# Kernel optimization log

Hardware: AMD Instinct MI355X
Metric: run time of the kernel (lower is better)

The kernel has to match this reference:

```python
import jax, jax.numpy as jnp
import numpy as np


def _elem_mlp(x, w1, b1, w2, b2):
    # elementwise 1 -> N -> 1 ReLU MLP (distilled exp / inv approximators)
    h = jax.nn.relu(x[..., None] * w1[:, 0] + b1)  # [..., N]
    return jnp.einsum('...n,n->...', h, w2[0]) + b2[0]


def setup_inputs() -> dict:
    key = jax.random.key(0)
    ks = jax.random.split(key, 13)
    T, S, B, D = 8, 512, 8, 512
    NE, NI = 32, 64
    f = jnp.float32
    inp = {
        'sx': jax.random.normal(ks[0], (T, S, B, D), f) * 0.1,
        'q_proj_weight': jax.random.normal(ks[1], (D, D), f) / np.sqrt(D),
        'k_proj_weight': jax.random.normal(ks[2], (D, D), f) / np.sqrt(D),
        'q_proj_bias': jax.random.normal(ks[3], (D,), f) * 0.02,
        'k_proj_bias': jax.random.normal(ks[4], (D,), f) * 0.02,
        'exp_w1': jax.random.normal(ks[5], (NE, 1), f),
        'exp_b1': jax.random.normal(ks[6], (NE,), f) * 0.1,
        'exp_w2': jax.random.normal(ks[7], (1, NE), f) / np.sqrt(NE),
        'exp_b2': jax.random.normal(ks[8], (1,), f) * 0.01,
        'inv_w1': jax.random.normal(ks[9], (NI, 1), f),
        'inv_b1': jax.random.normal(ks[10], (NI,), f) * 0.1,
        'inv_w2': jax.random.normal(ks[11], (1, NI), f) / np.sqrt(NI),
        'inv_b2': jax.random.normal(ks[12], (1,), f) * 0.01,
        'num_heads': 8,
    }
    return inp


def reference(sx, q_proj_weight, k_proj_weight, q_proj_bias, k_proj_bias,
              exp_w1, exp_b1, exp_w2, exp_b2,
              inv_w1, inv_b1, inv_w2, inv_b2, num_heads):
    T, S, B, D = sx.shape
    H = num_heads
    hd = D // H
    scale = 1.0 / np.sqrt(hd)

    def proj(x_t, W, b):
        # [S, B, D] -> [B*H, S, hd]
        y = x_t @ W.T + b
        return y.reshape(S, B * H, hd).transpose(1, 0, 2)

    def step(carry, x_t):
        sum_q, sum_k, sum_p = carry
        sq = proj(x_t, q_proj_weight, q_proj_bias)
        sk = proj(x_t, k_proj_weight, k_proj_bias)
        sum_q = sum_q + sq
        # sp_t = sum_q @ sk^T + sq @ sum_k^T (sum_k updated AFTER, per snn_qk_product)
        sp = (jnp.einsum('bsh,bth->bst', sum_q, sk)
              + jnp.einsum('bsh,bth->bst', sq, sum_k)) * scale
        sum_k = sum_k + sk
        return (sum_q, sum_k, sum_p + sp), None

    z_qk = jnp.zeros((B * H, S, hd), sx.dtype)
    z_p = jnp.zeros((B * H, S, S), sx.dtype)
    (sum_q, sum_k, sum_p), _ = jax.lax.scan(step, (z_qk, z_qk, z_p), sx)

    p = sum_p / T  # time-averaged accumulated QK product

    # fit_softmax: distilled-MLP softmax approximation
    tmax = p[:, :, 0:1]
    tp = jnp.minimum(p - (tmax - 1.0), 3.0)
    x_up = jnp.where(tp > -20.0,
                     _elem_mlp(tp, exp_w1, exp_b1, exp_w2, exp_b2), 0.0)
    partition = x_up.sum(-1, keepdims=True)
    p_inv = _elem_mlp(partition, inv_w1, inv_b1, inv_w2, inv_b2)
    out = x_up * p_inv
    partition_p2 = out.sum(-1, keepdims=True)
    p_inv2 = _elem_mlp(partition_p2, inv_w1, inv_b1, inv_w2, inv_b2)
    out2 = jnp.where(partition_p2 > 1.5, out * p_inv2, out)
    return out2
```

## Files before the change

kernel.cpp:

```cpp
#include <hip/hip_runtime.h>


#define T_  8
#define NE_ 32
#define NI_ 64

#define LUT_N   2048
#define LUT_LO  -20.0f
#define LUT_HI  3.0f
#define LUT_INVW (LUT_N / (LUT_HI - LUT_LO))
#define LUT_W    ((LUT_HI - LUT_LO) / LUT_N)

typedef __attribute__((ext_vector_type(8))) short bf16x8;
typedef __attribute__((ext_vector_type(4))) float f32x4;
typedef __attribute__((ext_vector_type(4))) unsigned int u32x4;

#define XS_OFF 0u
#define WQ_OFF 2097152u
#define WK_OFF 2359296u
#define QB_OFF 2621440u
#define KB_OFF 4718592u
#define LUT_OFF 6815744u

__device__ inline unsigned short f2bf(float f) {
  union { float f; unsigned u; } v; v.f = f;
  unsigned r = v.u + 0x7FFFu + ((v.u >> 16) & 1u);
  return (unsigned short)(r >> 16);
}

__device__ inline void gload16(const void* g, void* l) {
  __builtin_amdgcn_global_load_lds(
      (const __attribute__((address_space(1))) void*)g,
      (__attribute__((address_space(3))) void*)l, 16, 0, 0);
}

__device__ inline bf16x8 lds_read_swz(const unsigned short* base, int row, int byteoff) {
  int addr = row * 128 + (byteoff ^ ((row & 7) << 4));
  return *(const bf16x8*)((const char*)base + addr);
}

__device__ inline float invmlp4(float x, const float* __restrict__ w1,
                                const float* __restrict__ b1,
                                const float* __restrict__ w2, float b2) {
  float a0 = b2, a1 = 0.f, a2 = 0.f, a3 = 0.f;
#pragma unroll
  for (int n = 0; n < NI_; n += 4) {
    a0 += w2[n + 0] * fmaxf(x * w1[n + 0] + b1[n + 0], 0.0f);
    a1 += w2[n + 1] * fmaxf(x * w1[n + 1] + b1[n + 1], 0.0f);
    a2 += w2[n + 2] * fmaxf(x * w1[n + 2] + b1[n + 2], 0.0f);
    a3 += w2[n + 3] * fmaxf(x * w1[n + 3] + b1[n + 3], 0.0f);
  }
  return (a0 + a1) + (a2 + a3);
}

__device__ inline float expmlp_exact(float t, const float* __restrict__ w1,
                                     const float* __restrict__ b1,
                                     const float* __restrict__ w2, float b2) {
  float a = b2;
#pragma unroll
  for (int n = 0; n < NE_; n++) a += w2[n] * fmaxf(t * w1[n] + b1[n], 0.0f);
  return a;
}

__global__ __launch_bounds__(256) void k_pre(
    const float* __restrict__ sx, const float* __restrict__ wq,
    const float* __restrict__ wk, const float* __restrict__ ew1,
    const float* __restrict__ eb1, const float* __restrict__ ew2,
    const float* __restrict__ eb2p,
    unsigned short* __restrict__ xs, unsigned short* __restrict__ wqb,
    unsigned short* __restrict__ wkb, float2* __restrict__ lut) {
  int bx = blockIdx.x, tid = threadIdx.x;
  if (bx < 2048) {
    size_t i = ((size_t)bx * 256 + tid) * 4;
    f32x4 a = __builtin_nontemporal_load((const f32x4*)(sx + i));
#pragma unroll
    for (int t = 1; t < T_; t++) {
      f32x4 v = __builtin_nontemporal_load((const f32x4*)(sx + (size_t)t * 2097152 + i));
      a += v;
    }
    ushort4 o; o.x = f2bf(a[0]); o.y = f2bf(a[1]); o.z = f2bf(a[2]); o.w = f2bf(a[3]);
    *(ushort4*)(xs + i) = o;
  } else if (bx < 2560) {
    const float* src = (bx < 2304) ? wq : wk;
    unsigned short* dst = (bx < 2304) ? wqb : wkb;
    int base = (bx < 2304) ? 2048 : 2304;
    size_t i = ((size_t)(bx - base) * 256 + tid) * 4;
    float4 a = *(const float4*)(src + i);
    ushort4 o; o.x = f2bf(a.x); o.y = f2bf(a.y); o.z = f2bf(a.z); o.w = f2bf(a.w);
    *(ushort4*)(dst + i) = o;
  } else {
    int i = (bx - 2560) * 256 + tid;
    if (i < LUT_N) {
      float b2 = eb2p[0];
      float tl = fmaf((float)i, LUT_W, LUT_LO);
      float th = fmaf((float)(i + 1), LUT_W, LUT_LO);
      float el = expmlp_exact(tl, ew1, eb1, ew2, b2);
      float eh = expmlp_exact(th, ew1, eb1, ew2, b2);
      float ap = eh - el;
      float bp = fmaf(-ap, (float)i, el);
      lut[i] = make_float2(ap, bp);
    }
  }
}

__global__ __launch_bounds__(256, 2) void k_proj(
    const unsigned short* __restrict__ xs, const unsigned short* __restrict__ wb,
    const float* __restrict__ bq, const float* __restrict__ bk,
    unsigned short* __restrict__ outb) {
  __shared__ unsigned short As[64 * 64];
  __shared__ unsigned short Bs[128 * 64];
  int tid = threadIdx.x;
  int lane = tid & 63, w = tid >> 6;
  int r0 = blockIdx.x * 64;
  int c0 = blockIdx.y * 128;
  int z = blockIdx.z;
  const unsigned short* W = wb + (size_t)z * 262144;
  const float* bias = z ? bk : bq;
  unsigned short* dst = outb + (size_t)z * 2097152;
  float sc = z ? 1.0f : (1.0f / 64.0f);

  int rgrp = lane >> 4, cl = lane & 15;
  int r0w = (w >> 1) * 32, c0w = (w & 1) * 64;

  f32x4 acc[2][4];
  f32x4 zero = {0.f, 0.f, 0.f, 0.f};
#pragma unroll
  for (int m = 0; m < 2; m++)
#pragma unroll
    for (int n = 0; n < 4; n++) acc[m][n] = zero;

  int rl = lane >> 3, slot = lane & 7;

  for (int kt = 0; kt < 8; kt++) {
    int k0 = kt * 64;
#pragma unroll
    for (int i = 0; i < 2; i++) {
      int chunk = w * 2 + i;
      int r = chunk * 8 + rl;
      int sw = (slot ^ (r & 7)) * 8;
      gload16(xs + (size_t)(r0 + r) * 512 + k0 + sw, (char*)As + chunk * 1024);
    }
#pragma unroll
    for (int i = 0; i < 4; i++) {
      int chunk = w * 4 + i;
      int r = chunk * 8 + rl;
      int sw = (slot ^ (r & 7)) * 8;
      gload16(W + (size_t)(c0 + r) * 512 + k0 + sw, (char*)Bs + chunk * 1024);
    }
    __syncthreads();
#pragma unroll
    for (int kb = 0; kb < 2; kb++) {
      bf16x8 af[2], bfr[4];
#pragma unroll
      for (int m = 0; m < 2; m++) af[m] = lds_read_swz(As, r0w + 16 * m + cl, kb * 64 + rgrp * 16);
#pragma unroll
      for (int n = 0; n < 4; n++) bfr[n] = lds_read_swz(Bs, c0w + 16 * n + cl, kb * 64 + rgrp * 16);
#pragma unroll
      for (int m = 0; m < 2; m++)
#pragma unroll
        for (int n = 0; n < 4; n++)
          acc[m][n] = __builtin_amdgcn_mfma_f32_16x16x32_bf16(af[m], bfr[n], acc[m][n], 0, 0, 0);
    }
    __syncthreads();
  }

  unsigned short* Os = Bs;
#pragma unroll
  for (int n = 0; n < 4; n++) {
    int cgl = c0w + 16 * n + cl;
    float bv = 8.0f * bias[c0 + cgl];
    int hl = cgl >> 6, dh = cgl & 63;
    int hh = dh >> 5, rg2 = (dh >> 3) & 3, jj = dh & 7;
#pragma unroll
    for (int m = 0; m < 2; m++) {
#pragma unroll
      for (int j = 0; j < 4; j++) {
        int rgl = r0w + 16 * m + rgrp * 4 + j;
        int b = rgl & 7, clsl = rgl >> 3;
        Os[((((b * 2 + hl) * 2 + hh) * 4 + rg2) * 8 + clsl) * 8 + jj] =
            f2bf((acc[m][n][j] + bv) * sc);
      }
    }
  }
  __syncthreads();

  int cb = blockIdx.x >> 1;
  int clsbase = (blockIdx.x & 1) * 8;
  int h0 = c0 >> 6;
#pragma unroll
  for (int i2 = 0; i2 < 4; i2++) {
    int unit = i2 * 256 + tid;
    int clsl = unit & 7, rg2 = (unit >> 3) & 3, hh = (unit >> 5) & 1;
    int hl = (unit >> 6) & 1, b = unit >> 7;
    int bh = b * 8 + h0 + hl;
    size_t du = ((size_t)((bh * 32 + cb) * 2 + hh)) * 512 + (rg2 * 16 + clsbase + clsl) * 8;
    *(u32x4*)(dst + du) = *(const u32x4*)(Os + unit * 8);
  }
}

__global__ __launch_bounds__(256, 4) void k_attn(
    const unsigned short* __restrict__ qb, const unsigned short* __restrict__ kb,
    const float2* __restrict__ lutg,
    const float* __restrict__ iw1, const float* __restrict__ ib1,
    const float* __restrict__ iw2, const float* __restrict__ ib2p,
    float* __restrict__ out) {
  __shared__ float2 Lut[LUT_N];
  __shared__ float s_part[4][16];
  __shared__ float s_fac[16];

  int tid = threadIdx.x;
  int lane = tid & 63, w = tid >> 6;
  int i = blockIdx.x;
  int xcd = i & 7, j2 = i >> 3;
  int bh = xcd * 8 + (j2 >> 5);
  int rb = j2 & 31;
  int rgrp = lane >> 4, cl = lane & 15;

#pragma unroll
  for (int c = 0; c < 4; c++) {
    int chunk = w * 4 + c;
    gload16((const char*)lutg + chunk * 1024 + lane * 16, (char*)Lut + chunk * 1024);
  }

  const char* Qb = (const char*)qb + (size_t)((bh * 32 + rb) * 2) * 1024;
  bf16x8 aF0 = *(const bf16x8*)(Qb + lane * 16);
  bf16x8 aF1 = *(const bf16x8*)(Qb + 1024 + lane * 16);

  const char* Kbase = (const char*)kb + (size_t)(bh * 32) * 2048;
  f32x4 zero = {0.f, 0.f, 0.f, 0.f};

  float tm1[4];
  {
    bf16x8 b0 = *(const bf16x8*)(Kbase + lane * 16);
    bf16x8 b1 = *(const bf16x8*)(Kbase + 1024 + lane * 16);
    f32x4 p0 = __builtin_amdgcn_mfma_f32_16x16x32_bf16(aF0, b0, zero, 0, 0, 0);
    p0 = __builtin_amdgcn_mfma_f32_16x16x32_bf16(aF1, b1, p0, 0, 0, 0);
    int src = lane & 48;
#pragma unroll
    for (int j = 0; j < 4; j++) tm1[j] = __shfl(p0[j], src) - 1.0f;
  }

  f32x4 acc[8];
#pragma unroll
  for (int f = 0; f < 8; f++) {
    const char* Kb = Kbase + (size_t)(w * 8 + f) * 2048;
    bf16x8 b0 = *(const bf16x8*)(Kb + lane * 16);
    bf16x8 b1 = *(const bf16x8*)(Kb + 1024 + lane * 16);
    acc[f] = __builtin_amdgcn_mfma_f32_16x16x32_bf16(aF0, b0, zero, 0, 0, 0);
    acc[f] = __builtin_amdgcn_mfma_f32_16x16x32_bf16(aF1, b1, acc[f], 0, 0, 0);
  }

  __syncthreads();

  const float C0 = -LUT_LO * LUT_INVW;
  float cj[4];
#pragma unroll
  for (int j = 0; j < 4; j++) cj[j] = fmaf(-tm1[j], LUT_INVW, C0);

  float rowsum[4] = {0.f, 0.f, 0.f, 0.f};
#pragma unroll
  for (int f = 0; f < 8; f++) {
#pragma unroll
    for (int j = 0; j < 4; j++) {
      float u0 = fmaf(acc[f][j], LUT_INVW, cj[j]);
      float u = fminf(fmaxf(u0, 0.0f), (float)LUT_N);
      int bi = (int)u;
      bi = min(bi, LUT_N - 1);
      float2 ab = Lut[bi];
      float xu = fmaf(ab.x, u, ab.y);
      xu = (u0 > 0.0f) ? xu : 0.0f;
      acc[f][j] = xu;
      rowsum[j] += xu;
    }
  }

#pragma unroll
  for (int j = 0; j < 4; j++) {
    float s = rowsum[j];
    s += __shfl_xor(s, 1);
    s += __shfl_xor(s, 2);
    s += __shfl_xor(s, 4);
    s += __shfl_xor(s, 8);
    if (cl == 0) s_part[w][rgrp * 4 + j] = s;
  }
  __syncthreads();

  if (tid < 16) {
    float part = s_part[0][tid] + s_part[1][tid] + s_part[2][tid] + s_part[3][tid];
    float b2 = ib2p[0];
    float fac = invmlp4(part, iw1, ib1, iw2, b2);
    float pp2 = part * fac;
    if (pp2 > 1.5f) fac *= invmlp4(pp2, iw1, ib1, iw2, b2);
    s_fac[tid] = fac;
  }
  __syncthreads();

  float* outb = out + ((size_t)bh * 512 + rb * 16) * 512;
#pragma unroll
  for (int j = 0; j < 4; j++) {
    int row = rgrp * 4 + j;
    float fac = s_fac[row];
#pragma unroll
    for (int f = 0; f < 8; f++)
      __builtin_nontemporal_store(acc[f][j] * fac,
          &outb[(size_t)row * 512 + w * 128 + 16 * f + cl]);
  }
}

extern "C" void kernel_launch(void* const* d_in, const int* in_sizes, int n_in,
                              void* d_out, int out_size, void* d_ws, size_t ws_size,
                              hipStream_t stream) {
  (void)in_sizes; (void)n_in; (void)out_size; (void)ws_size;
  const float* sx  = (const float*)d_in[0];
  const float* wq  = (const float*)d_in[1];
  const float* wk  = (const float*)d_in[2];
  const float* bq  = (const float*)d_in[3];
  const float* bk  = (const float*)d_in[4];
  const float* ew1 = (const float*)d_in[5];
  const float* eb1 = (const float*)d_in[6];
  const float* ew2 = (const float*)d_in[7];
  const float* eb2 = (const float*)d_in[8];
  const float* iw1 = (const float*)d_in[9];
  const float* ib1 = (const float*)d_in[10];
  const float* iw2 = (const float*)d_in[11];
  const float* ib2 = (const float*)d_in[12];
  unsigned short* wsu = (unsigned short*)d_ws;
  float2* lut = (float2*)(wsu + LUT_OFF);
  float* out = (float*)d_out;

  k_pre<<<2568, 256, 0, stream>>>(sx, wq, wk, ew1, eb1, ew2, eb2,
                                  wsu + XS_OFF, wsu + WQ_OFF, wsu + WK_OFF, lut);
  k_proj<<<dim3(64, 4, 2), 256, 0, stream>>>(wsu + XS_OFF, wsu + WQ_OFF, bq, bk, wsu + QB_OFF);
  k_attn<<<2048, 256, 0, stream>>>(wsu + QB_OFF, wsu + KB_OFF, lut,
                                   iw1, ib1, iw2, ib2, out);
}
```

Baseline: 56.62 us.

## Transpose QK MFMA operands so each lane owns a row; vectorize stores, split inverse MLP

Swaps the A/B operands of the QK MFMA so each lane's four accumulator values belong to one query row across four adjacent columns, instead of four rows. The row max offset and row sum then each need one scalar per lane, and the sum reduces with two cross-lane shuffles instead of four per row. The inverse-MLP normalisation, previously run serially by 16 threads behind an extra barrier, is now split across all lanes with a shuffle reduction. This removes a __syncthreads and lets the output be written as 16-byte vector nontemporal stores. The trade-off is that every lane now computes the second inverse MLP whether or not the threshold is met.

```diff
diff --git a/kernel.cpp b/kernel.cpp
--- a/kernel.cpp
+++ b/kernel.cpp
@@ -37,20 +37,6 @@
 __device__ inline bf16x8 lds_read_swz(const unsigned short* base, int row, int byteoff) {
   int addr = row * 128 + (byteoff ^ ((row & 7) << 4));
   return *(const bf16x8*)((const char*)base + addr);
-}
-
-__device__ inline float invmlp4(float x, const float* __restrict__ w1,
-                                const float* __restrict__ b1,
-                                const float* __restrict__ w2, float b2) {
-  float a0 = b2, a1 = 0.f, a2 = 0.f, a3 = 0.f;
-#pragma unroll
-  for (int n = 0; n < NI_; n += 4) {
-    a0 += w2[n + 0] * fmaxf(x * w1[n + 0] + b1[n + 0], 0.0f);
-    a1 += w2[n + 1] * fmaxf(x * w1[n + 1] + b1[n + 1], 0.0f);
-    a2 += w2[n + 2] * fmaxf(x * w1[n + 2] + b1[n + 2], 0.0f);
-    a3 += w2[n + 3] * fmaxf(x * w1[n + 3] + b1[n + 3], 0.0f);
-  }
-  return (a0 + a1) + (a2 + a3);
 }
 
 __device__ inline float expmlp_exact(float t, const float* __restrict__ w1,
@@ -206,7 +192,6 @@
     float* __restrict__ out) {
   __shared__ float2 Lut[LUT_N];
   __shared__ float s_part[4][16];
-  __shared__ float s_fac[16];
 
   int tid = threadIdx.x;
   int lane = tid & 63, w = tid >> 6;
@@ -223,46 +208,42 @@
   }
 
   const char* Qb = (const char*)qb + (size_t)((bh * 32 + rb) * 2) * 1024;
-  bf16x8 aF0 = *(const bf16x8*)(Qb + lane * 16);
-  bf16x8 aF1 = *(const bf16x8*)(Qb + 1024 + lane * 16);
+  bf16x8 qF0 = *(const bf16x8*)(Qb + lane * 16);
+  bf16x8 qF1 = *(const bf16x8*)(Qb + 1024 + lane * 16);
 
   const char* Kbase = (const char*)kb + (size_t)(bh * 32) * 2048;
   f32x4 zero = {0.f, 0.f, 0.f, 0.f};
 
-  float tm1[4];
+  float tm1;
   {
-    bf16x8 b0 = *(const bf16x8*)(Kbase + lane * 16);
-    bf16x8 b1 = *(const bf16x8*)(Kbase + 1024 + lane * 16);
-    f32x4 p0 = __builtin_amdgcn_mfma_f32_16x16x32_bf16(aF0, b0, zero, 0, 0, 0);
-    p0 = __builtin_amdgcn_mfma_f32_16x16x32_bf16(aF1, b1, p0, 0, 0, 0);
-    int src = lane & 48;
-#pragma unroll
-    for (int j = 0; j < 4; j++) tm1[j] = __shfl(p0[j], src) - 1.0f;
+    bf16x8 k0 = *(const bf16x8*)(Kbase + lane * 16);
+    bf16x8 k1 = *(const bf16x8*)(Kbase + 1024 + lane * 16);
+    f32x4 p0 = __builtin_amdgcn_mfma_f32_16x16x32_bf16(k0, qF0, zero, 0, 0, 0);
+    p0 = __builtin_amdgcn_mfma_f32_16x16x32_bf16(k1, qF1, p0, 0, 0, 0);
+    tm1 = __shfl(p0[0], cl) - 1.0f;
   }
 
   f32x4 acc[8];
 #pragma unroll
   for (int f = 0; f < 8; f++) {
     const char* Kb = Kbase + (size_t)(w * 8 + f) * 2048;
-    bf16x8 b0 = *(const bf16x8*)(Kb + lane * 16);
-    bf16x8 b1 = *(const bf16x8*)(Kb + 1024 + lane * 16);
-    acc[f] = __builtin_amdgcn_mfma_f32_16x16x32_bf16(aF0, b0, zero, 0, 0, 0);
-    acc[f] = __builtin_amdgcn_mfma_f32_16x16x32_bf16(aF1, b1, acc[f], 0, 0, 0);
+    bf16x8 k0 = *(const bf16x8*)(Kb + lane * 16);
+    bf16x8 k1 = *(const bf16x8*)(Kb + 1024 + lane * 16);
+    acc[f] = __builtin_amdgcn_mfma_f32_16x16x32_bf16(k0, qF0, zero, 0, 0, 0);
+    acc[f] = __builtin_amdgcn_mfma_f32_16x16x32_bf16(k1, qF1, acc[f], 0, 0, 0);
   }
 
   __syncthreads();
 
   const float C0 = -LUT_LO * LUT_INVW;
-  float cj[4];
-#pragma unroll
-  for (int j = 0; j < 4; j++) cj[j] = fmaf(-tm1[j], LUT_INVW, C0);
-
-  float rowsum[4] = {0.f, 0.f, 0.f, 0.f};
+  float cj = fmaf(-tm1, LUT_INVW, C0);
+
+  float rowsum = 0.0f;
 #pragma unroll
   for (int f = 0; f < 8; f++) {
 #pragma unroll
     for (int j = 0; j < 4; j++) {
-      float u0 = fmaf(acc[f][j], LUT_INVW, cj[j]);
+      float u0 = fmaf(acc[f][j], LUT_INVW, cj);
       float u = fminf(fmaxf(u0, 0.0f), (float)LUT_N);
       int bi = (int)u;
       bi = min(bi, LUT_N - 1);
@@ -270,40 +251,46 @@
       float xu = fmaf(ab.x, u, ab.y);
       xu = (u0 > 0.0f) ? xu : 0.0f;
       acc[f][j] = xu;
-      rowsum[j] += xu;
-    }
-  }
-
-#pragma unroll
-  for (int j = 0; j < 4; j++) {
-    float s = rowsum[j];
-    s += __shfl_xor(s, 1);
-    s += __shfl_xor(s, 2);
-    s += __shfl_xor(s, 4);
-    s += __shfl_xor(s, 8);
-    if (cl == 0) s_part[w][rgrp * 4 + j] = s;
-  }
+      rowsum += xu;
+    }
+  }
+
+  rowsum += __shfl_xor(rowsum, 16);
+  rowsum += __shfl_xor(rowsum, 32);
+  if (lane < 16) s_part[w][lane] = rowsum;
   __syncthreads();
 
-  if (tid < 16) {
-    float part = s_part[0][tid] + s_part[1][tid] + s_part[2][tid] + s_part[3][tid];
-    float b2 = ib2p[0];
-    float fac = invmlp4(part, iw1, ib1, iw2, b2);
-    float pp2 = part * fac;
-    if (pp2 > 1.5f) fac *= invmlp4(pp2, iw1, ib1, iw2, b2);
-    s_fac[tid] = fac;
-  }
-  __syncthreads();
-
-  float* outb = out + ((size_t)bh * 512 + rb * 16) * 512;
-#pragma unroll
-  for (int j = 0; j < 4; j++) {
-    int row = rgrp * 4 + j;
-    float fac = s_fac[row];
-#pragma unroll
-    for (int f = 0; f < 8; f++)
-      __builtin_nontemporal_store(acc[f][j] * fac,
-          &outb[(size_t)row * 512 + w * 128 + 16 * f + cl]);
+  float part = s_part[0][cl] + s_part[1][cl] + s_part[2][cl] + s_part[3][cl];
+
+  float b2 = ib2p[0];
+  float a = 0.0f;
+#pragma unroll
+  for (int nn = 0; nn < 16; nn++) {
+    int n = rgrp * 16 + nn;
+    a += iw2[n] * fmaxf(part * iw1[n] + ib1[n], 0.0f);
+  }
+  a += __shfl_xor(a, 16);
+  a += __shfl_xor(a, 32);
+  float pinv = a + b2;
+  float pp2 = part * pinv;
+  float b = 0.0f;
+#pragma unroll
+  for (int nn = 0; nn < 16; nn++) {
+    int n = rgrp * 16 + nn;
+    b += iw2[n] * fmaxf(pp2 * iw1[n] + ib1[n], 0.0f);
+  }
+  b += __shfl_xor(b, 16);
+  b += __shfl_xor(b, 32);
+  float pinv2 = b + b2;
+  float fac = (pp2 > 1.5f) ? pinv * pinv2 : pinv;
+
+  float* outb = out + ((size_t)(bh * 512 + rb * 16 + cl)) * 512 + w * 128 + rgrp * 4;
+#pragma unroll
+  for (int f = 0; f < 8; f++) {
+    f32x4 v;
+#pragma unroll
+    for (int j = 0; j < 4; j++) v[j] = acc[f][j] * fac;
+    __builtin_nontemporal_store(v, (f32x4*)(outb + f * 16));
   }
 }
 
```

Result: faster. 54.15 us, median of 2 (-4.4%).
